# Kernel optimization log

Hardware: AMD Instinct MI355X
Metric: run time of the kernel (lower is better)

## Reference

```python
import jax, jax.numpy as jnp
import numpy as np

B, NUM_RX, NUM_CHIRPS, SAMPLES = 16, 4, 64, 256
D_BINS, R_BINS = 64, 256


def _conv3d(x, w, b, pad):
    y = jax.lax.conv_general_dilated(x, w, (1, 1, 1), pad,
                                     dimension_numbers=('NCDHW', 'OIDHW', 'NCDHW'))
    return y + b[None, :, None, None, None]


def _conv2d(x, w, b, pad):
    y = jax.lax.conv_general_dilated(x, w, (1, 1), pad,
                                     dimension_numbers=('NCHW', 'OIHW', 'NCHW'))
    return y + b[None, :, None, None]


def _bn2(x, s, t):
    return x * s[None, :, None, None] + t[None, :, None, None]


def _bn3(x, s, t):
    return x * s[None, :, None, None, None] + t[None, :, None, None, None]


def _upsample_bilinear_ac(x, oh, ow):
    # torch Upsample(mode='bilinear', align_corners=True)
    _, _, h, w = x.shape
    ph = jnp.linspace(0.0, h - 1.0, oh)
    pw = jnp.linspace(0.0, w - 1.0, ow)
    h0 = jnp.clip(jnp.floor(ph).astype(jnp.int32), 0, h - 1)
    h1 = jnp.clip(h0 + 1, 0, h - 1)
    fh = ph - h0
    w0 = jnp.clip(jnp.floor(pw).astype(jnp.int32), 0, w - 1)
    w1 = jnp.clip(w0 + 1, 0, w - 1)
    fw = pw - w0
    x = x[:, :, h0, :] * (1.0 - fh)[None, None, :, None] + x[:, :, h1, :] * fh[None, None, :, None]
    x = x[:, :, :, w0] * (1.0 - fw) + x[:, :, :, w1] * fw
    return x


def setup_inputs() -> dict:
    ks = iter(jax.random.split(jax.random.key(0), 80))

    def nrm(shape, s=0.05):
        return s * jax.random.normal(next(ks), shape, dtype=jnp.float32)

    inp = {'x': jax.random.normal(next(ks), (B, NUM_RX, NUM_CHIRPS, SAMPLES, 2), dtype=jnp.float32)}

    def conv(name, shape):
        inp[name + '_w'] = nrm(shape)
        inp[name + '_b'] = nrm((shape[0],))

    def bn(name, n):  # BatchNorm in inference form folded to scale/shift
        inp[name + '_s'] = 1.0 + nrm((n,), 0.1)
        inp[name + '_t'] = nrm((n,), 0.1)

    conv('tc1', (16, 2, 1, 1, 3)); bn('tc1', 16)
    conv('tc2', (32, 16, 1, 1, 3)); bn('tc2', 32)
    conv('rx', (32, 32, NUM_RX, 1, 1)); bn('rx', 32)
    conv('cc1', (64, 32 * NUM_CHIRPS, 3, 3)); bn('cc1', 64)
    conv('cc2', (64, 64, 3, 3)); bn('cc2', 64)
    conv('rd1', (128, 64, 3, 3)); bn('rd1', 128)
    conv('rd2', (128, 128, 3, 3)); bn('rd2', 128)
    conv('up1', (64, 128, 3, 3)); bn('up1', 64)
    conv('up2', (32, 64, 3, 3)); bn('up2', 32)
    conv('up3', (1, 32, 1, 1))
    inp['wr'] = jax.random.normal(next(ks), (SAMPLES, R_BINS, 2), dtype=jnp.float32)
    inp['wd'] = jax.random.normal(next(ks), (NUM_CHIRPS, D_BINS, 2), dtype=jnp.float32)
    return inp


def reference(x, tc1_w, tc1_b, tc1_s, tc1_t, tc2_w, tc2_b, tc2_s, tc2_t,
              rx_w, rx_b, rx_s, rx_t, cc1_w, cc1_b, cc1_s, cc1_t,
              cc2_w, cc2_b, cc2_s, cc2_t, rd1_w, rd1_b, rd1_s, rd1_t,
              rd2_w, rd2_b, rd2_s, rd2_t, up1_w, up1_b, up1_s, up1_t,
              up2_w, up2_b, up2_s, up2_t, up3_w, up3_b, wr, wd):
    r = jax.nn.relu
    p3 = [(0, 0), (0, 0), (1, 1)]
    p2 = [(1, 1), (1, 1)]
    h = jnp.transpose(x, (0, 4, 1, 2, 3))                      # [B,2,RX,C,S]
    h = r(_bn3(_conv3d(h, tc1_w, tc1_b, p3), tc1_s, tc1_t))
    h = r(_bn3(_conv3d(h, tc2_w, tc2_b, p3), tc2_s, tc2_t))
    h = r(_bn3(_conv3d(h, rx_w, rx_b, [(0, 0)] * 3), rx_s, rx_t))[:, :, 0]  # [B,32,C,S]
    h = h.reshape(h.shape[0], -1, SAMPLES)[:, :, None, :]      # [B,32*C,1,S]
    h = r(_bn2(_conv2d(h, cc1_w, cc1_b, p2), cc1_s, cc1_t))
    h = r(_bn2(_conv2d(h, cc2_w, cc2_b, p2), cc2_s, cc2_t))
    h = r(_bn2(_conv2d(h, rd1_w, rd1_b, p2), rd1_s, rd1_t))
    h = r(_bn2(_conv2d(h, rd2_w, rd2_b, p2), rd2_s, rd2_t))
    h = _upsample_bilinear_ac(h, D_BINS, R_BINS)               # [B,128,D,R]
    h = r(_bn2(_conv2d(h, up1_w, up1_b, p2), up1_s, up1_t))
    h = r(_bn2(_conv2d(h, up2_w, up2_b, p2), up2_s, up2_t))
    h = jax.nn.sigmoid(_conv2d(h, up3_w, up3_b, [(0, 0), (0, 0)]))  # [B,1,D,R]
    # learnable_fft (input is real: x_imag = 0), loops -> two batched matmuls
    xr = h[:, 0]                                               # [B,D,R]
    rr = jnp.einsum('bcs,sr->bcr', xr, wr[:, :, 0])            # range DFT, real
    ri = jnp.einsum('bcs,sr->bcr', xr, wr[:, :, 1])            # range DFT, imag
    rdr = jnp.einsum('bcr,cd->bdr', rr, wd[:, :, 0]) - jnp.einsum('bcr,cd->bdr', ri, wd[:, :, 1])
    rdi = jnp.einsum('bcr,cd->bdr', rr, wd[:, :, 1]) + jnp.einsum('bcr,cd->bdr', ri, wd[:, :, 0])
    mag = jnp.sqrt(rdr * rdr + rdi * rdi) / (NUM_CHIRPS * SAMPLES)
    out = jnp.clip(h + 0.1 * mag[:, None], 0.0, 1.0)
    return jnp.transpose(out, (0, 2, 3, 1))                    # [B,D,R,1]
```

## Files before the change

### kernel.cpp

```cpp
#include <hip/hip_runtime.h>
#include <math.h>

#define OFF_A      0u
#define OFF_P      8388608u
#define OFF_WCC1   10485760u
#define OFF_BCC1   10878976u
#define OFF_WCC2   10879040u
#define OFF_BCC2   10895424u
#define OFF_WRD1   10895488u
#define OFF_BRD1   10928256u
#define OFF_WRD2   10928384u
#define OFF_BRD2   10993920u
#define OFF_WUP1   10994048u
#define OFF_BUP1   11092352u
#define OFF_WUP2   11092416u
#define OFF_BUP2   11215296u
#define OFF_WRX    11215328u
#define OFF_W1F    11219424u
#define OFF_B1F    11219520u
#define OFF_W2F    11219536u
#define OFF_B2F    11221072u
#define OFF_BRXF   11221104u
#define OFF_R      0u
#define OFF_H      524288u

__device__ __forceinline__ void fma4(float4& a, const float4& x, float w) {
  a.x = fmaf(x.x, w, a.x); a.y = fmaf(x.y, w, a.y);
  a.z = fmaf(x.z, w, a.z); a.w = fmaf(x.w, w, a.w);
}

__global__ __launch_bounds__(256) void k_repack_front(
    const float* __restrict__ tc1_w, const float* __restrict__ tc1_b, const float* __restrict__ tc1_s, const float* __restrict__ tc1_t,
    const float* __restrict__ tc2_w, const float* __restrict__ tc2_b, const float* __restrict__ tc2_s, const float* __restrict__ tc2_t,
    const float* __restrict__ rx_w, const float* __restrict__ rx_b, const float* __restrict__ rx_s, const float* __restrict__ rx_t,
    float* __restrict__ ws)
{
  const int tid = blockIdx.x * blockDim.x + threadIdx.x;
  const int nth = gridDim.x * blockDim.x;
  for (int i = tid; i < 96; i += nth) ws[OFF_W1F + i] = tc1_w[i] * tc1_s[i/6];
  for (int i = tid; i < 16; i += nth) ws[OFF_B1F + i] = tc1_b[i]*tc1_s[i] + tc1_t[i];
  for (int i = tid; i < 1536; i += nth) {
    int oc = i & 31, r = i >> 5, k = r % 3, ic = r / 3;
    ws[OFF_W2F + i] = tc2_w[oc*48 + ic*3 + k] * tc2_s[oc];
  }
  for (int i = tid; i < 32; i += nth) ws[OFF_B2F + i] = tc2_b[i]*tc2_s[i] + tc2_t[i];
  for (int i = tid; i < 4096; i += nth) {
    int oc = i & 31, ic = (i >> 5) & 31, rxi = i >> 10;
    ws[OFF_WRX + i] = rx_w[(oc*32 + ic)*4 + rxi] * rx_s[oc];
  }
  for (int i = tid; i < 32; i += nth) ws[OFF_BRXF + i] = rx_b[i]*rx_s[i] + rx_t[i];
}

__global__ __launch_bounds__(256, 4) void k_front(
    const float* __restrict__ x, const float* __restrict__ ws_c, float* __restrict__ ws,
    const float* __restrict__ cc1_w, const float* __restrict__ cc1_b, const float* __restrict__ cc1_s, const float* __restrict__ cc1_t,
    const float* __restrict__ cc2_w, const float* __restrict__ cc2_b, const float* __restrict__ cc2_s, const float* __restrict__ cc2_t,
    const float* __restrict__ rd1_w, const float* __restrict__ rd1_b, const float* __restrict__ rd1_s, const float* __restrict__ rd1_t,
    const float* __restrict__ rd2_w, const float* __restrict__ rd2_b, const float* __restrict__ rd2_s, const float* __restrict__ rd2_t,
    const float* __restrict__ up1_w, const float* __restrict__ up1_b, const float* __restrict__ up1_s, const float* __restrict__ up1_t,
    const float* __restrict__ up2_w, const float* __restrict__ up2_b, const float* __restrict__ up2_s, const float* __restrict__ up2_t,
    float* __restrict__ A)
{
  __shared__ float t1s[16][258];
  const int tid = threadIdx.x;

  if (blockIdx.x < 64) {
    const int t = blockIdx.x * 256 + tid;
    const int nth = 64 * 256;
    for (int i = t; i < 2048*192; i += nth) {
      int c = i / 192, r = i - c*192, k = r >> 6, oc = r & 63;
      ws[OFF_WCC1 + i] = cc1_w[((oc*2048 + c)*3 + 1)*3 + k] * cc1_s[oc];
    }
    for (int i = t; i < 64; i += nth) ws[OFF_BCC1 + i] = cc1_b[i]*cc1_s[i] + cc1_t[i];
    for (int i = t; i < 64*64; i += nth) {
      int oc = i & 63, ic = i >> 6;
      float4 v;
      v.x = cc2_w[(oc*64 + ic)*9 + 3] * cc2_s[oc];
      v.y = cc2_w[(oc*64 + ic)*9 + 4] * cc2_s[oc];
      v.z = cc2_w[(oc*64 + ic)*9 + 5] * cc2_s[oc];
      v.w = 0.f;
      ((float4*)(ws + OFF_WCC2))[i] = v;
    }
    for (int i = t; i < 64; i += nth) ws[OFF_BCC2 + i] = cc2_b[i]*cc2_s[i] + cc2_t[i];
    for (int i = t; i < 64*128; i += nth) {
      int oc = i & 127, ic = i >> 7;
      float4 v;
      v.x = rd1_w[(oc*64 + ic)*9 + 3] * rd1_s[oc];
      v.y = rd1_w[(oc*64 + ic)*9 + 4] * rd1_s[oc];
      v.z = rd1_w[(oc*64 + ic)*9 + 5] * rd1_s[oc];
      v.w = 0.f;
      ((float4*)(ws + OFF_WRD1))[i] = v;
    }
    for (int i = t; i < 128; i += nth) ws[OFF_BRD1 + i] = rd1_b[i]*rd1_s[i] + rd1_t[i];
    for (int i = t; i < 128*128; i += nth) {
      int oc = i & 127, ic = i >> 7;
      float4 v;
      v.x = rd2_w[(oc*128 + ic)*9 + 3] * rd2_s[oc];
      v.y = rd2_w[(oc*128 + ic)*9 + 4] * rd2_s[oc];
      v.z = rd2_w[(oc*128 + ic)*9 + 5] * rd2_s[oc];
      v.w = 0.f;
      ((float4*)(ws + OFF_WRD2))[i] = v;
    }
    for (int i = t; i < 128; i += nth) ws[OFF_BRD2 + i] = rd2_b[i]*rd2_s[i] + rd2_t[i];
    for (int i = t; i < 3*128*64; i += nth) {
      int oc = i & 63, ic = (i >> 6) & 127, v = i >> 13;
      const int m = (v == 0) ? 6 : (v == 1) ? 7 : 3;
      float4 o = make_float4(0.f, 0.f, 0.f, 0.f);
      for (int kh = 0; kh < 3; ++kh)
        if ((m >> kh) & 1) {
          o.x += up1_w[((oc*128 + ic)*3 + kh)*3 + 0];
          o.y += up1_w[((oc*128 + ic)*3 + kh)*3 + 1];
          o.z += up1_w[((oc*128 + ic)*3 + kh)*3 + 2];
        }
      o.x *= up1_s[oc]; o.y *= up1_s[oc]; o.z *= up1_s[oc];
      ((float4*)(ws + OFF_WUP1))[i] = o;
    }
    for (int i = t; i < 64; i += nth) ws[OFF_BUP1 + i] = up1_b[i]*up1_s[i] + up1_t[i];
    for (int i = t; i < 5*3*64*32; i += nth) {
      int oc = i & 31, ic = (i >> 5) & 63, tt = i >> 11;
      int src = tt % 3, v = tt / 3;
      const int MASKS[15] = {2,4,0,  1,6,0,  0,7,0,  0,3,4,  0,1,2};
      const int m = MASKS[v*3 + src];
      float4 o = make_float4(0.f, 0.f, 0.f, 0.f);
      for (int kh = 0; kh < 3; ++kh)
        if ((m >> kh) & 1) {
          o.x += up2_w[((oc*64 + ic)*3 + kh)*3 + 0];
          o.y += up2_w[((oc*64 + ic)*3 + kh)*3 + 1];
          o.z += up2_w[((oc*64 + ic)*3 + kh)*3 + 2];
        }
      o.x *= up2_s[oc]; o.y *= up2_s[oc]; o.z *= up2_s[oc];
      ((float4*)(ws + OFF_WUP2))[i] = o;
    }
    for (int i = t; i < 32; i += nth) ws[OFF_BUP2 + i] = up2_b[i]*up2_s[i] + up2_t[i];
    return;
  }

  const int bb = blockIdx.x - 64;
  const int b = bb >> 6, chirp = bb & 63;
  const int s = tid;

  if (tid < 32) { int o = tid & 15; int c = (tid >> 4) ? 257 : 0; t1s[o][c] = 0.f; }

  const float* w1f  = ws_c + OFF_W1F;
  const float* b1f  = ws_c + OFF_B1F;
  const float* w2f  = ws_c + OFF_W2F;
  const float* b2f  = ws_c + OFF_B2F;
  const float* wrxf = ws_c + OFF_WRX;
  const float* brxf = ws_c + OFF_BRXF;

  float acc[32];
  #pragma unroll
  for (int j = 0; j < 32; ++j) acc[j] = 0.f;

  #pragma unroll 1
  for (int rxi = 0; rxi < 4; ++rxi) {
    {
      const float2* xb2 = (const float2*)(x + ((size_t)(((b*4 + rxi)*64 + chirp)*256) << 1));
      float2 xm = xb2[s];
      float2 xl = xb2[(s == 0) ? 0 : (s - 1)];
      float2 xr = xb2[(s == 255) ? 255 : (s + 1)];
      if (s == 0)   { xl.x = 0.f; xl.y = 0.f; }
      if (s == 255) { xr.x = 0.f; xr.y = 0.f; }
      #pragma unroll 4
      for (int o = 0; o < 16; ++o) {
        const float* w = w1f + o*6;
        float v = b1f[o];
        v = fmaf(xl.x, w[0], v);
        v = fmaf(xm.x, w[1], v);
        v = fmaf(xr.x, w[2], v);
        v = fmaf(xl.y, w[3], v);
        v = fmaf(xm.y, w[4], v);
        v = fmaf(xr.y, w[5], v);
        t1s[o][s+1] = fmaxf(v, 0.f);
      }
    }
    __syncthreads();

    float t2[32];
    #pragma unroll
    for (int j = 0; j < 32; ++j) t2[j] = b2f[j];
    #pragma unroll 2
    for (int ic = 0; ic < 16; ++ic) {
      float tl = t1s[ic][s];
      float tm = t1s[ic][s+1];
      float tr = t1s[ic][s+2];
      const float* w = w2f + ic*96;
      #pragma unroll
      for (int oc = 0; oc < 32; ++oc)
        t2[oc] = fmaf(tl, w[oc], fmaf(tm, w[32+oc], fmaf(tr, w[64+oc], t2[oc])));
    }
    #pragma unroll
    for (int j = 0; j < 32; ++j) t2[j] = fmaxf(t2[j], 0.f);

    const float* wr0 = wrxf + rxi*1024;
    #pragma unroll 4
    for (int ic = 0; ic < 32; ++ic) {
      float tv = t2[ic];
      const float* w = wr0 + ic*32;
      #pragma unroll
      for (int oc = 0; oc < 32; ++oc)
        acc[oc] = fmaf(tv, w[oc], acc[oc]);
    }
    __syncthreads();
  }

  #pragma unroll 4
  for (int oc = 0; oc < 32; ++oc) {
    float v = fmaxf(acc[oc] + brxf[oc], 0.f);
    A[(size_t)((b*2048 + oc*64 + chirp)*256) + s] = v;
  }
}

__global__ __launch_bounds__(128) void k_cc1(
    const float* __restrict__ A, const float* __restrict__ wp, float* __restrict__ P)
{
  __shared__ __align__(16) float As[256][20];
  const int tid = threadIdx.x;
  const int ks = blockIdx.x & 7;
  const int stile = (blockIdx.x >> 3) & 15;
  const int b = blockIdx.x >> 7;
  const int s0 = stile * 16;
  const int ocq = tid & 15;
  const int sg = tid >> 4;
  const int sb = sg * 2;
  const int cbase = ks * 256;

  for (int i = tid; i < 256*20; i += 128) {
    int c = i / 20, si = i - c*20;
    int sA = s0 - 1 + si;
    float v = 0.f;
    if (si < 18 && sA >= 0 && sA < 256)
      v = A[(size_t)(b*2048 + cbase + c)*256 + sA];
    As[c][si] = v;
  }
  __syncthreads();

  float4 acc0 = make_float4(0.f,0.f,0.f,0.f);
  float4 acc1 = make_float4(0.f,0.f,0.f,0.f);
  const float4* w4 = (const float4*)wp;
  #pragma unroll 4
  for (int c = 0; c < 256; ++c) {
    const float4* wc = w4 + (size_t)(cbase + c)*48 + ocq;
    float4 wk0 = wc[0];
    float4 wk1 = wc[16];
    float4 wk2 = wc[32];
    float2 a01 = *(const float2*)&As[c][sb];
    float2 a23 = *(const float2*)&As[c][sb + 2];
    fma4(acc0, wk0, a01.x); fma4(acc0, wk1, a01.y); fma4(acc0, wk2, a23.x);
    fma4(acc1, wk0, a01.y); fma4(acc1, wk1, a23.x); fma4(acc1, wk2, a23.y);
  }
  float* Pk = P + ((size_t)(ks*16 + b)*256)*64;
  *(float4*)&Pk[(size_t)(s0 + sb + 0)*64 + ocq*4] = acc0;
  *(float4*)&Pk[(size_t)(s0 + sb + 1)*64 + ocq*4] = acc1;
}

__global__ __launch_bounds__(256) void k_mid(
    const float* __restrict__ P, const float* __restrict__ bcc1,
    const float* __restrict__ wcc2, const float* __restrict__ bcc2,
    const float* __restrict__ wrd1, const float* __restrict__ brd1,
    const float* __restrict__ wrd2, const float* __restrict__ brd2,
    float* __restrict__ R)
{
  __shared__ __align__(16) float c1s[64][20];
  __shared__ __align__(16) float c2s[64][20];
  __shared__ __align__(16) float r1s[128][12];
  const int tid = threadIdx.x;
  const int b = blockIdx.x >> 5;
  const int s0 = (blockIdx.x & 31) * 8;
  const float4* wc2 = (const float4*)wcc2;
  const float4* wr1 = (const float4*)wrd1;
  const float4* wr2 = (const float4*)wrd2;

  for (int i = tid; i < 64*14; i += 256) {
    int ic = i & 63, si = i >> 6;
    int sA = s0 - 3 + si;
    float v = 0.f;
    if (sA >= 0 && sA < 256) {
      float a = bcc1[ic];
      #pragma unroll
      for (int ksp = 0; ksp < 8; ++ksp)
        a += P[((size_t)(ksp*16 + b)*256 + sA)*64 + ic];
      v = fmaxf(a, 0.f);
    }
    c1s[ic][si] = v;
  }
  __syncthreads();

  {
    const int g = tid >> 6, oc = tid & 63;
    if (g < 3) {
      float bb = bcc2[oc];
      float4 acc = make_float4(bb, bb, bb, bb);
      for (int ic = 0; ic < 64; ++ic) {
        float4 w = wc2[ic*64 + oc];
        float4 ca = *(const float4*)&c1s[ic][g*4];
        float2 cb = *(const float2*)&c1s[ic][g*4 + 4];
        acc.x = fmaf(ca.x,w.x, fmaf(ca.y,w.y, fmaf(ca.z,w.z, acc.x)));
        acc.y = fmaf(ca.y,w.x, fmaf(ca.z,w.y, fmaf(ca.w,w.z, acc.y)));
        acc.z = fmaf(ca.z,w.x, fmaf(ca.w,w.y, fmaf(cb.x,w.z, acc.z)));
        acc.w = fmaf(ca.w,w.x, fmaf(cb.x,w.y, fmaf(cb.y,w.z, acc.w)));
      }
      c2s[oc][g*4+0] = fmaxf(acc.x, 0.f);
      c2s[oc][g*4+1] = fmaxf(acc.y, 0.f);
      c2s[oc][g*4+2] = fmaxf(acc.z, 0.f);
      c2s[oc][g*4+3] = fmaxf(acc.w, 0.f);
    } else {
      int oc2 = tid - 192;
      c2s[oc2][12] = 0.f;
      c2s[oc2][13] = 0.f;
    }
  }
  __syncthreads();

  for (int it = tid; it < 384; it += 256) {
    const int oc = it & 127, g = it >> 7;
    float bb = brd1[oc];
    float4 acc = make_float4(bb, bb, bb, bb);
    for (int ic = 0; ic < 64; ++ic) {
      float4 w = wr1[ic*128 + oc];
      float4 ca = *(const float4*)&c2s[ic][g*4];
      float2 cb = *(const float2*)&c2s[ic][g*4 + 4];
      acc.x = fmaf(ca.x,w.x, fmaf(ca.y,w.y, fmaf(ca.z,w.z, acc.x)));
      acc.y = fmaf(ca.y,w.x, fmaf(ca.z,w.y, fmaf(ca.w,w.z, acc.y)));
      acc.z = fmaf(ca.z,w.x, fmaf(ca.w,w.y, fmaf(cb.x,w.z, acc.z)));
      acc.w = fmaf(ca.w,w.x, fmaf(cb.x,w.y, fmaf(cb.y,w.z, acc.w)));
    }
    if (g*4 + 0 < 12) r1s[oc][g*4+0] = fmaxf(acc.x, 0.f);
    if (g*4 + 1 < 12) r1s[oc][g*4+1] = fmaxf(acc.y, 0.f);
    if (g*4 + 2 < 12) r1s[oc][g*4+2] = fmaxf(acc.z, 0.f);
    if (g*4 + 3 < 12) r1s[oc][g*4+3] = fmaxf(acc.w, 0.f);
  }
  __syncthreads();

  {
    const int g = tid >> 7, oc = tid & 127;
    float bb = brd2[oc];
    float4 acc = make_float4(bb, bb, bb, bb);
    for (int ic = 0; ic < 128; ++ic) {
      float4 w = wr2[ic*128 + oc];
      float4 ca = *(const float4*)&r1s[ic][g*4];
      float2 cb = *(const float2*)&r1s[ic][g*4 + 4];
      acc.x = fmaf(ca.x,w.x, fmaf(ca.y,w.y, fmaf(ca.z,w.z, acc.x)));
      acc.y = fmaf(ca.y,w.x, fmaf(ca.z,w.y, fmaf(ca.w,w.z, acc.y)));
      acc.z = fmaf(ca.z,w.x, fmaf(ca.w,w.y, fmaf(cb.x,w.z, acc.z)));
      acc.w = fmaf(ca.w,w.x, fmaf(cb.x,w.y, fmaf(cb.y,w.z, acc.w)));
    }
    int s = s0 + g*4;
    R[((size_t)b*256 + s+0)*128 + oc] = fmaxf(acc.x, 0.f);
    R[((size_t)b*256 + s+1)*128 + oc] = fmaxf(acc.y, 0.f);
    R[((size_t)b*256 + s+2)*128 + oc] = fmaxf(acc.z, 0.f);
    R[((size_t)b*256 + s+3)*128 + oc] = fmaxf(acc.w, 0.f);
  }
}

__global__ __launch_bounds__(192) void k_up(
    const float* __restrict__ R,
    const float* __restrict__ wup1, const float* __restrict__ bup1,
    const float* __restrict__ wup2, const float* __restrict__ bup2,
    const float* __restrict__ up3_w, const float* __restrict__ up3_b,
    float* __restrict__ H)
{
  __shared__ __align__(16) float Rs[128][12];
  __shared__ __align__(16) float u1s[3][64][12];
  __shared__ float u2s[5][32][9];
  const int tid = threadIdx.x;
  const int b = blockIdx.x >> 5;
  const int s0 = (blockIdx.x & 31) * 8;

  for (int i = tid; i < 128*12; i += 192) {
    int ic = i & 127, si = i >> 7;
    int sA = s0 - 2 + si;
    Rs[ic][si] = (sA >= 0 && sA < 256) ? R[((size_t)b*256 + sA)*128 + ic] : 0.f;
  }
  __syncthreads();

  if (tid < 96) {
    const int vi = tid >> 5, ocp = tid & 31;
    const int oc0 = ocp*2, oc1 = ocp*2 + 1;
    const float4* w4 = (const float4*)wup1;
    float a0[10], a1[10];
    float bb0 = bup1[oc0], bb1 = bup1[oc1];
    #pragma unroll
    for (int p = 0; p < 10; ++p) { a0[p] = bb0; a1[p] = bb1; }
    for (int ic = 0; ic < 128; ++ic) {
      float4 w0 = w4[(vi*128 + ic)*64 + oc0];
      float4 w1 = w4[(vi*128 + ic)*64 + oc1];
      float4 ra = *(const float4*)&Rs[ic][0];
      float4 rb = *(const float4*)&Rs[ic][4];
      float4 rc = *(const float4*)&Rs[ic][8];
      float r[12] = {ra.x,ra.y,ra.z,ra.w, rb.x,rb.y,rb.z,rb.w, rc.x,rc.y,rc.z,rc.w};
      #pragma unroll
      for (int p = 0; p < 10; ++p) {
        a0[p] = fmaf(r[p],w0.x, fmaf(r[p+1],w0.y, fmaf(r[p+2],w0.z, a0[p])));
        a1[p] = fmaf(r[p],w1.x, fmaf(r[p+1],w1.y, fmaf(r[p+2],w1.z, a1[p])));
      }
    }
    #pragma unroll
    for (int p = 0; p < 10; ++p) {
      u1s[vi][oc0][p] = fmaxf(a0[p], 0.f);
      u1s[vi][oc1][p] = fmaxf(a1[p], 0.f);
    }
    u1s[vi][oc0][10] = 0.f; u1s[vi][oc0][11] = 0.f;
    u1s[vi][oc1][10] = 0.f; u1s[vi][oc1][11] = 0.f;
  }
  __syncthreads();

  if (tid < 80) {
    const int v = tid >> 4, ocp = tid & 15;
    const int oc0 = ocp*2, oc1 = ocp*2 + 1;
    const float4* w4 = (const float4*)wup2;
    float a0[8], a1[8];
    float bb0 = bup2[oc0], bb1 = bup2[oc1];
    #pragma unroll
    for (int p = 0; p < 8; ++p) { a0[p] = bb0; a1[p] = bb1; }
    for (int src = 0; src < 3; ++src)
      for (int ic = 0; ic < 64; ++ic) {
        float4 w0 = w4[((v*3 + src)*64 + ic)*32 + oc0];
        float4 w1 = w4[((v*3 + src)*64 + ic)*32 + oc1];
        float4 ua = *(const float4*)&u1s[src][ic][0];
        float4 ub = *(const float4*)&u1s[src][ic][4];
        float2 uc = *(const float2*)&u1s[src][ic][8];
        float r[10] = {ua.x,ua.y,ua.z,ua.w, ub.x,ub.y,ub.z,ub.w, uc.x,uc.y};
        #pragma unroll
        for (int p = 0; p < 8; ++p) {
          a0[p] = fmaf(r[p],w0.x, fmaf(r[p+1],w0.y, fmaf(r[p+2],w0.z, a0[p])));
          a1[p] = fmaf(r[p],w1.x, fmaf(r[p+1],w1.y, fmaf(r[p+2],w1.z, a1[p])));
        }
      }
    #pragma unroll
    for (int p = 0; p < 8; ++p) {
      u2s[v][oc0][p] = fmaxf(a0[p], 0.f);
      u2s[v][oc1][p] = fmaxf(a1[p], 0.f);
    }
  }
  __syncthreads();

  if (tid < 40) {
    int v = tid >> 3, j = tid & 7;
    float a = up3_b[0];
    for (int ic = 0; ic < 32; ++ic)
      a = fmaf(u2s[v][ic][j], up3_w[ic], a);
    H[(size_t)(b*5 + v)*256 + s0 + j] = 1.f / (1.f + expf(-a));
  }
}

__global__ __launch_bounds__(256) void k_spec(
    const float* __restrict__ H, const float* __restrict__ wr, const float* __restrict__ wd,
    float* __restrict__ out)
{
  __shared__ float hs[5][256];
  __shared__ float S0[64], S1[64];
  __shared__ float wds[4][64][2];
  __shared__ float ps[16][16][10];
  __shared__ float rred[16][10];
  const int tid = threadIdx.x;
  const int b = blockIdx.x >> 4;
  const int rt = blockIdx.x & 15;
  const int r0 = rt * 16;

  for (int i = tid; i < 1280; i += 256) hs[i >> 8][i & 255] = H[(size_t)b*1280 + i];
  if (tid < 64) {
    const float2* wd2 = (const float2*)wd;
    float a0 = 0.f, a1 = 0.f;
    for (int c = 2; c <= 61; ++c) {
      float2 v = wd2[c*64 + tid];
      a0 += v.x; a1 += v.y;
    }
    S0[tid] = a0; S1[tid] = a1;
  }
  for (int i = tid; i < 512; i += 256) {
    int row = i >> 7, rem = i & 127, d = rem >> 1, comp = rem & 1;
    int c = (row < 2) ? row : (60 + row);
    wds[row][d][comp] = wd[(c*64 + d)*2 + comp];
  }
  __syncthreads();

  {
    const int rl = tid & 15;
    const int sq = tid >> 4;
    const int r = r0 + rl;
    float rr[5] = {0,0,0,0,0}, ri[5] = {0,0,0,0,0};
    const float2* wr2p = (const float2*)wr;
    for (int s = sq*16; s < sq*16 + 16; ++s) {
      float2 w = wr2p[s*256 + r];
      #pragma unroll
      for (int k = 0; k < 5; ++k) {
        float hv = hs[k][s];
        rr[k] = fmaf(hv, w.x, rr[k]);
        ri[k] = fmaf(hv, w.y, ri[k]);
      }
    }
    #pragma unroll
    for (int k = 0; k < 5; ++k) {
      ps[sq][rl][k]     = rr[k];
      ps[sq][rl][5 + k] = ri[k];
    }
  }
  __syncthreads();

  if (tid < 160) {
    const int rl = tid & 15, k = tid >> 4;
    float a = 0.f;
    #pragma unroll
    for (int sq = 0; sq < 16; ++sq) a += ps[sq][rl][k];
    rred[rl][k] = a;
  }
  __syncthreads();

  {
    const int rl = tid & 15, dg = tid >> 4;
    const int r = r0 + rl;
    float Rr[5], Ri[5];
    #pragma unroll
    for (int k = 0; k < 5; ++k) { Rr[k] = rred[rl][k]; Ri[k] = rred[rl][5 + k]; }
    for (int dd = 0; dd < 4; ++dd) {
      int d = dg*4 + dd;
      float w0r = wds[0][d][0], w0i = wds[0][d][1];
      float w1r = wds[1][d][0], w1i = wds[1][d][1];
      float w2r = wds[2][d][0], w2i = wds[2][d][1];
      float w3r = wds[3][d][0], w3i = wds[3][d][1];
      float s0v = S0[d], s1v = S1[d];
      float rdr = Rr[0]*w0r + Rr[1]*w1r + Rr[2]*s0v + Rr[3]*w2r + Rr[4]*w3r
                - Ri[0]*w0i - Ri[1]*w1i - Ri[2]*s1v - Ri[3]*w2i - Ri[4]*w3i;
      float rdi = Rr[0]*w0i + Rr[1]*w1i + Rr[2]*s1v + Rr[3]*w2i + Rr[4]*w3i
                + Ri[0]*w0r + Ri[1]*w1r + Ri[2]*s0v + Ri[3]*w2r + Ri[4]*w3r;
      float mag = sqrtf(rdr*rdr + rdi*rdi) * (1.0f / 16384.0f);
      int v = (d == 0) ? 0 : (d == 1) ? 1 : (d <= 61) ? 2 : ((d == 62) ? 3 : 4);
      float o = hs[v][r] + 0.1f * mag;
      out[(size_t)b*16384 + d*256 + r] = fminf(fmaxf(o, 0.f), 1.f);
    }
  }
}

extern "C" void kernel_launch(void* const* d_in, const int* in_sizes, int n_in,
                              void* d_out, int out_size, void* d_ws, size_t ws_size,
                              hipStream_t stream)
{
  const float* x     = (const float*)d_in[0];
  const float* tc1_w = (const float*)d_in[1];  const float* tc1_b = (const float*)d_in[2];
  const float* tc1_s = (const float*)d_in[3];  const float* tc1_t = (const float*)d_in[4];
  const float* tc2_w = (const float*)d_in[5];  const float* tc2_b = (const float*)d_in[6];
  const float* tc2_s = (const float*)d_in[7];  const float* tc2_t = (const float*)d_in[8];
  const float* rx_w  = (const float*)d_in[9];  const float* rx_b  = (const float*)d_in[10];
  const float* rx_s  = (const float*)d_in[11]; const float* rx_t  = (const float*)d_in[12];
  const float* cc1_w = (const float*)d_in[13]; const float* cc1_b = (const float*)d_in[14];
  const float* cc1_s = (const float*)d_in[15]; const float* cc1_t = (const float*)d_in[16];
  const float* cc2_w = (const float*)d_in[17]; const float* cc2_b = (const float*)d_in[18];
  const float* cc2_s = (const float*)d_in[19]; const float* cc2_t = (const float*)d_in[20];
  const float* rd1_w = (const float*)d_in[21]; const float* rd1_b = (const float*)d_in[22];
  const float* rd1_s = (const float*)d_in[23]; const float* rd1_t = (const float*)d_in[24];
  const float* rd2_w = (const float*)d_in[25]; const float* rd2_b = (const float*)d_in[26];
  const float* rd2_s = (const float*)d_in[27]; const float* rd2_t = (const float*)d_in[28];
  const float* up1_w = (const float*)d_in[29]; const float* up1_b = (const float*)d_in[30];
  const float* up1_s = (const float*)d_in[31]; const float* up1_t = (const float*)d_in[32];
  const float* up2_w = (const float*)d_in[33]; const float* up2_b = (const float*)d_in[34];
  const float* up2_s = (const float*)d_in[35]; const float* up2_t = (const float*)d_in[36];
  const float* up3_w = (const float*)d_in[37]; const float* up3_b = (const float*)d_in[38];
  const float* wr    = (const float*)d_in[39];
  const float* wd    = (const float*)d_in[40];
  float* ws  = (float*)d_ws;
  float* out = (float*)d_out;

  k_repack_front<<<8, 256, 0, stream>>>(tc1_w, tc1_b, tc1_s, tc1_t,
                                        tc2_w, tc2_b, tc2_s, tc2_t,
                                        rx_w, rx_b, rx_s, rx_t, ws);
  k_front<<<1088, 256, 0, stream>>>(x, ws, ws,
                                    cc1_w, cc1_b, cc1_s, cc1_t,
                                    cc2_w, cc2_b, cc2_s, cc2_t,
                                    rd1_w, rd1_b, rd1_s, rd1_t,
                                    rd2_w, rd2_b, rd2_s, rd2_t,
                                    up1_w, up1_b, up1_s, up1_t,
                                    up2_w, up2_b, up2_s, up2_t,
                                    ws + OFF_A);
  k_cc1<<<2048, 128, 0, stream>>>(ws + OFF_A, ws + OFF_WCC1, ws + OFF_P);
  k_mid<<<512, 256, 0, stream>>>(ws + OFF_P, ws + OFF_BCC1,
                                 ws + OFF_WCC2, ws + OFF_BCC2,
                                 ws + OFF_WRD1, ws + OFF_BRD1,
                                 ws + OFF_WRD2, ws + OFF_BRD2, ws + OFF_R);
  k_up<<<512, 192, 0, stream>>>(ws + OFF_R, ws + OFF_WUP1, ws + OFF_BUP1,
                                ws + OFF_WUP2, ws + OFF_BUP2, up3_w, up3_b, ws + OFF_H);
  k_spec<<<256, 256, 0, stream>>>(ws + OFF_H, wr, wd, out);
}
```

Measured before the change: 415.4 us.

## Retile cc1 conv to per-channel threads with 8 outputs and repack weights

Repacks the cc1 weights as float4 per (channel, output channel), padded from 3 to 4 taps. k_cc1 now uses 256-thread blocks covering 32 positions, with each thread computing 8 consecutive positions for one output channel, so it does one weight load per channel instead of three. In k_up, the up1 and up2 stages spread one output channel per thread across more threads, and unroll pragmas are added to several inner loops. The trade-offs are larger weight storage, scalar stores into P, and more register pressure.

```diff
diff --git a/kernel.cpp b/kernel.cpp
--- a/kernel.cpp
+++ b/kernel.cpp
@@ -4,23 +4,23 @@
 #define OFF_A      0u
 #define OFF_P      8388608u
 #define OFF_WCC1   10485760u
-#define OFF_BCC1   10878976u
-#define OFF_WCC2   10879040u
-#define OFF_BCC2   10895424u
-#define OFF_WRD1   10895488u
-#define OFF_BRD1   10928256u
-#define OFF_WRD2   10928384u
-#define OFF_BRD2   10993920u
-#define OFF_WUP1   10994048u
-#define OFF_BUP1   11092352u
-#define OFF_WUP2   11092416u
-#define OFF_BUP2   11215296u
-#define OFF_WRX    11215328u
-#define OFF_W1F    11219424u
-#define OFF_B1F    11219520u
-#define OFF_W2F    11219536u
-#define OFF_B2F    11221072u
-#define OFF_BRXF   11221104u
+#define OFF_BCC1   11010048u
+#define OFF_WCC2   11010112u
+#define OFF_BCC2   11026496u
+#define OFF_WRD1   11026560u
+#define OFF_BRD1   11059328u
+#define OFF_WRD2   11059456u
+#define OFF_BRD2   11124992u
+#define OFF_WUP1   11125120u
+#define OFF_BUP1   11223424u
+#define OFF_WUP2   11223488u
+#define OFF_BUP2   11346368u
+#define OFF_WRX    11346400u
+#define OFF_W1F    11350496u
+#define OFF_B1F    11350592u
+#define OFF_W2F    11350608u
+#define OFF_B2F    11352144u
+#define OFF_BRXF   11352176u
 #define OFF_R      0u
 #define OFF_H      524288u
 
@@ -67,9 +67,9 @@
   if (blockIdx.x < 64) {
     const int t = blockIdx.x * 256 + tid;
     const int nth = 64 * 256;
-    for (int i = t; i < 2048*192; i += nth) {
-      int c = i / 192, r = i - c*192, k = r >> 6, oc = r & 63;
-      ws[OFF_WCC1 + i] = cc1_w[((oc*2048 + c)*3 + 1)*3 + k] * cc1_s[oc];
+    for (int i = t; i < 2048*64*4; i += nth) {
+      int k = i & 3, oc = (i >> 2) & 63, c2 = i >> 8;
+      ws[OFF_WCC1 + i] = (k < 3) ? cc1_w[((oc*2048 + c2)*3 + 1)*3 + k] * cc1_s[oc] : 0.f;
     }
     for (int i = t; i < 64; i += nth) ws[OFF_BCC1 + i] = cc1_b[i]*cc1_s[i] + cc1_t[i];
     for (int i = t; i < 64*64; i += nth) {
@@ -211,47 +211,58 @@
   }
 }
 
-__global__ __launch_bounds__(128) void k_cc1(
+__global__ __launch_bounds__(256) void k_cc1(
     const float* __restrict__ A, const float* __restrict__ wp, float* __restrict__ P)
 {
-  __shared__ __align__(16) float As[256][20];
+  __shared__ __align__(16) float As[256][36];
   const int tid = threadIdx.x;
   const int ks = blockIdx.x & 7;
-  const int stile = (blockIdx.x >> 3) & 15;
-  const int b = blockIdx.x >> 7;
-  const int s0 = stile * 16;
-  const int ocq = tid & 15;
-  const int sg = tid >> 4;
-  const int sb = sg * 2;
+  const int stile = (blockIdx.x >> 3) & 7;
+  const int b = blockIdx.x >> 6;
+  const int s0 = stile * 32;
+  const int oc = tid & 63;
+  const int sg = tid >> 6;
   const int cbase = ks * 256;
-
-  for (int i = tid; i < 256*20; i += 128) {
-    int c = i / 20, si = i - c*20;
+  const float4* w4 = (const float4*)wp;
+
+  for (int i = tid; i < 256*36; i += 256) {
+    int c = i / 36, si = i - c*36;
     int sA = s0 - 1 + si;
     float v = 0.f;
-    if (si < 18 && sA >= 0 && sA < 256)
+    if (si < 34 && sA >= 0 && sA < 256)
       v = A[(size_t)(b*2048 + cbase + c)*256 + sA];
     As[c][si] = v;
   }
   __syncthreads();
 
+  const int sb = sg * 8;
   float4 acc0 = make_float4(0.f,0.f,0.f,0.f);
   float4 acc1 = make_float4(0.f,0.f,0.f,0.f);
-  const float4* w4 = (const float4*)wp;
   #pragma unroll 4
   for (int c = 0; c < 256; ++c) {
-    const float4* wc = w4 + (size_t)(cbase + c)*48 + ocq;
-    float4 wk0 = wc[0];
-    float4 wk1 = wc[16];
-    float4 wk2 = wc[32];
-    float2 a01 = *(const float2*)&As[c][sb];
-    float2 a23 = *(const float2*)&As[c][sb + 2];
-    fma4(acc0, wk0, a01.x); fma4(acc0, wk1, a01.y); fma4(acc0, wk2, a23.x);
-    fma4(acc1, wk0, a01.y); fma4(acc1, wk1, a23.x); fma4(acc1, wk2, a23.y);
+    float4 w = w4[(size_t)(cbase + c)*64 + oc];
+    float4 a0 = *(const float4*)&As[c][sb];
+    float4 a1 = *(const float4*)&As[c][sb + 4];
+    float2 a2 = *(const float2*)&As[c][sb + 8];
+    acc0.x = fmaf(a0.x,w.x, fmaf(a0.y,w.y, fmaf(a0.z,w.z, acc0.x)));
+    acc0.y = fmaf(a0.y,w.x, fmaf(a0.z,w.y, fmaf(a0.w,w.z, acc0.y)));
+    acc0.z = fmaf(a0.z,w.x, fmaf(a0.w,w.y, fmaf(a1.x,w.z, acc0.z)));
+    acc0.w = fmaf(a0.w,w.x, fmaf(a1.x,w.y, fmaf(a1.y,w.z, acc0.w)));
+    acc1.x = fmaf(a1.x,w.x, fmaf(a1.y,w.y, fmaf(a1.z,w.z, acc1.x)));
+    acc1.y = fmaf(a1.y,w.x, fmaf(a1.z,w.y, fmaf(a1.w,w.z, acc1.y)));
+    acc1.z = fmaf(a1.z,w.x, fmaf(a1.w,w.y, fmaf(a2.x,w.z, acc1.z)));
+    acc1.w = fmaf(a1.w,w.x, fmaf(a2.x,w.y, fmaf(a2.y,w.z, acc1.w)));
   }
   float* Pk = P + ((size_t)(ks*16 + b)*256)*64;
-  *(float4*)&Pk[(size_t)(s0 + sb + 0)*64 + ocq*4] = acc0;
-  *(float4*)&Pk[(size_t)(s0 + sb + 1)*64 + ocq*4] = acc1;
+  int s = s0 + sb;
+  Pk[(size_t)(s+0)*64 + oc] = acc0.x;
+  Pk[(size_t)(s+1)*64 + oc] = acc0.y;
+  Pk[(size_t)(s+2)*64 + oc] = acc0.z;
+  Pk[(size_t)(s+3)*64 + oc] = acc0.w;
+  Pk[(size_t)(s+4)*64 + oc] = acc1.x;
+  Pk[(size_t)(s+5)*64 + oc] = acc1.y;
+  Pk[(size_t)(s+6)*64 + oc] = acc1.z;
+  Pk[(size_t)(s+7)*64 + oc] = acc1.w;
 }
 
 __global__ __launch_bounds__(256) void k_mid(
@@ -291,6 +302,7 @@
     if (g < 3) {
       float bb = bcc2[oc];
       float4 acc = make_float4(bb, bb, bb, bb);
+      #pragma unroll 4
       for (int ic = 0; ic < 64; ++ic) {
         float4 w = wc2[ic*64 + oc];
         float4 ca = *(const float4*)&c1s[ic][g*4];
@@ -316,6 +328,7 @@
     const int oc = it & 127, g = it >> 7;
     float bb = brd1[oc];
     float4 acc = make_float4(bb, bb, bb, bb);
+    #pragma unroll 4
     for (int ic = 0; ic < 64; ++ic) {
       float4 w = wr1[ic*128 + oc];
       float4 ca = *(const float4*)&c2s[ic][g*4];
@@ -336,6 +349,7 @@
     const int g = tid >> 7, oc = tid & 127;
     float bb = brd2[oc];
     float4 acc = make_float4(bb, bb, bb, bb);
+    #pragma unroll 4
     for (int ic = 0; ic < 128; ++ic) {
       float4 w = wr2[ic*128 + oc];
       float4 ca = *(const float4*)&r1s[ic][g*4];
@@ -374,64 +388,52 @@
   }
   __syncthreads();
 
-  if (tid < 96) {
-    const int vi = tid >> 5, ocp = tid & 31;
-    const int oc0 = ocp*2, oc1 = ocp*2 + 1;
+  {
+    const int vi = tid >> 6, oc = tid & 63;
     const float4* w4 = (const float4*)wup1;
-    float a0[10], a1[10];
-    float bb0 = bup1[oc0], bb1 = bup1[oc1];
-    #pragma unroll
-    for (int p = 0; p < 10; ++p) { a0[p] = bb0; a1[p] = bb1; }
+    float a[10];
+    float bb = bup1[oc];
+    #pragma unroll
+    for (int p = 0; p < 10; ++p) a[p] = bb;
+    #pragma unroll 4
     for (int ic = 0; ic < 128; ++ic) {
-      float4 w0 = w4[(vi*128 + ic)*64 + oc0];
-      float4 w1 = w4[(vi*128 + ic)*64 + oc1];
+      float4 w = w4[(vi*128 + ic)*64 + oc];
       float4 ra = *(const float4*)&Rs[ic][0];
       float4 rb = *(const float4*)&Rs[ic][4];
       float4 rc = *(const float4*)&Rs[ic][8];
       float r[12] = {ra.x,ra.y,ra.z,ra.w, rb.x,rb.y,rb.z,rb.w, rc.x,rc.y,rc.z,rc.w};
       #pragma unroll
-      for (int p = 0; p < 10; ++p) {
-        a0[p] = fmaf(r[p],w0.x, fmaf(r[p+1],w0.y, fmaf(r[p+2],w0.z, a0[p])));
-        a1[p] = fmaf(r[p],w1.x, fmaf(r[p+1],w1.y, fmaf(r[p+2],w1.z, a1[p])));
-      }
-    }
-    #pragma unroll
-    for (int p = 0; p < 10; ++p) {
-      u1s[vi][oc0][p] = fmaxf(a0[p], 0.f);
-      u1s[vi][oc1][p] = fmaxf(a1[p], 0.f);
-    }
-    u1s[vi][oc0][10] = 0.f; u1s[vi][oc0][11] = 0.f;
-    u1s[vi][oc1][10] = 0.f; u1s[vi][oc1][11] = 0.f;
-  }
-  __syncthreads();
-
-  if (tid < 80) {
-    const int v = tid >> 4, ocp = tid & 15;
-    const int oc0 = ocp*2, oc1 = ocp*2 + 1;
+      for (int p = 0; p < 10; ++p)
+        a[p] = fmaf(r[p],w.x, fmaf(r[p+1],w.y, fmaf(r[p+2],w.z, a[p])));
+    }
+    #pragma unroll
+    for (int p = 0; p < 10; ++p) u1s[vi][oc][p] = fmaxf(a[p], 0.f);
+    u1s[vi][oc][10] = 0.f; u1s[vi][oc][11] = 0.f;
+  }
+  __syncthreads();
+
+  if (tid < 160) {
+    const int v = tid >> 5, oc = tid & 31;
     const float4* w4 = (const float4*)wup2;
-    float a0[8], a1[8];
-    float bb0 = bup2[oc0], bb1 = bup2[oc1];
-    #pragma unroll
-    for (int p = 0; p < 8; ++p) { a0[p] = bb0; a1[p] = bb1; }
-    for (int src = 0; src < 3; ++src)
+    float a[8];
+    float bb = bup2[oc];
+    #pragma unroll
+    for (int p = 0; p < 8; ++p) a[p] = bb;
+    for (int src = 0; src < 3; ++src) {
+      #pragma unroll 4
       for (int ic = 0; ic < 64; ++ic) {
-        float4 w0 = w4[((v*3 + src)*64 + ic)*32 + oc0];
-        float4 w1 = w4[((v*3 + src)*64 + ic)*32 + oc1];
+        float4 w = w4[((v*3 + src)*64 + ic)*32 + oc];
         float4 ua = *(const float4*)&u1s[src][ic][0];
         float4 ub = *(const float4*)&u1s[src][ic][4];
         float2 uc = *(const float2*)&u1s[src][ic][8];
         float r[10] = {ua.x,ua.y,ua.z,ua.w, ub.x,ub.y,ub.z,ub.w, uc.x,uc.y};
         #pragma unroll
-        for (int p = 0; p < 8; ++p) {
-          a0[p] = fmaf(r[p],w0.x, fmaf(r[p+1],w0.y, fmaf(r[p+2],w0.z, a0[p])));
-          a1[p] = fmaf(r[p],w1.x, fmaf(r[p+1],w1.y, fmaf(r[p+2],w1.z, a1[p])));
-        }
+        for (int p = 0; p < 8; ++p)
+          a[p] = fmaf(r[p],w.x, fmaf(r[p+1],w.y, fmaf(r[p+2],w.z, a[p])));
       }
-    #pragma unroll
-    for (int p = 0; p < 8; ++p) {
-      u2s[v][oc0][p] = fmaxf(a0[p], 0.f);
-      u2s[v][oc1][p] = fmaxf(a1[p], 0.f);
-    }
+    }
+    #pragma unroll
+    for (int p = 0; p < 8; ++p) u2s[v][oc][p] = fmaxf(a[p], 0.f);
   }
   __syncthreads();
 
@@ -572,7 +574,7 @@
                                     up1_w, up1_b, up1_s, up1_t,
                                     up2_w, up2_b, up2_s, up2_t,
                                     ws + OFF_A);
-  k_cc1<<<2048, 128, 0, stream>>>(ws + OFF_A, ws + OFF_WCC1, ws + OFF_P);
+  k_cc1<<<1024, 256, 0, stream>>>(ws + OFF_A, ws + OFF_WCC1, ws + OFF_P);
   k_mid<<<512, 256, 0, stream>>>(ws + OFF_P, ws + OFF_BCC1,
                                  ws + OFF_WCC2, ws + OFF_BCC2,
                                  ws + OFF_WRD1, ws + OFF_BRD1,
```

After: 339.1 us. 18.4% less time.
